# Kernel optimization log

Hardware: AMD Instinct MI355X
Metric: run time of the kernel (lower is better)

Reference implementation:

```python
import jax, jax.numpy as jnp
import numpy as np

H = 128  # DECODER_LAYERS[0]
LN_EPS = 1e-3  # keras LayerNormalization default epsilon


def setup_inputs() -> dict:
    key = jax.random.key(0)
    ks = jax.random.split(key, 12)
    N_POS, N_COL, D = 1024, 512, 128
    n_seq = 8
    s = 1.0 / np.sqrt(D)
    h = 1.0 / np.sqrt(H)
    return {
        "seq_feat": jax.random.normal(ks[0], (N_POS, D), jnp.float32),
        "col_feat": jax.random.normal(ks[1], (N_COL, D), jnp.float32),
        "sequence_lengths": jnp.full((n_seq,), N_POS // n_seq, dtype=jnp.int32),
        "Ws": jax.random.normal(ks[2], (D, H), jnp.float32) * s,
        "bs": jnp.zeros((H,), jnp.float32),
        "Wc": jax.random.normal(ks[3], (D, H), jnp.float32) * s,
        "bc": jnp.zeros((H,), jnp.float32),
        "Wm": jax.random.normal(ks[4], (H, H), jnp.float32) * h,
        "bm": jnp.zeros((H,), jnp.float32),
        "gamma": jnp.ones((H,), jnp.float32),
        "beta": jnp.zeros((H,), jnp.float32),
        "Wo": jax.random.normal(ks[5], (H, 1), jnp.float32) * h,
        "bo": jnp.zeros((1,), jnp.float32),
    }


def reference(seq_feat, col_feat, sequence_lengths, Ws, bs, Wc, bc, Wm, bm, gamma, beta, Wo, bo):
    N_POS = seq_feat.shape[0]
    N_COL = col_feat.shape[0]
    n_seq = sequence_lengths.shape[0]

    seq_dec = jax.nn.relu(seq_feat @ Ws + bs)   # [N_pos, H]
    col_dec = jax.nn.relu(col_feat @ Wc + bc)   # [N_col, H]

    # broadcast outer-sum: [N_pos, N_col, H]
    logits = seq_dec[:, None, :] + col_dec[None, :, :]

    # MLP([128]): single Dense (no activation) + LayerNorm
    hmid = logits @ Wm + bm
    mu = jnp.mean(hmid, axis=-1, keepdims=True)
    var = jnp.mean(jnp.square(hmid - mu), axis=-1, keepdims=True)
    hln = (hmid - mu) / jnp.sqrt(var + LN_EPS) * gamma + beta

    raw = (hln @ Wo + bo)[..., 0]               # [N_pos, N_col]
    exp_logits = jnp.exp(raw)

    # column-axis normalization (softmax over last axis)
    M_c = exp_logits / jnp.sum(exp_logits, axis=-1, keepdims=True)

    # segment-ragged normalization over positions, per sequence
    segment_ids = jnp.repeat(jnp.arange(n_seq, dtype=jnp.int32), sequence_lengths,
                             total_repeat_length=N_POS)
    seg = jax.ops.segment_sum(exp_logits, segment_ids, num_segments=n_seq)  # [n_seq, N_col]
    M_s = exp_logits / seg[segment_ids]

    return M_c + M_s - M_c * M_s
```

## Files before the change

### kernel.cpp

```cpp
#include <hip/hip_runtime.h>

#define HDIM 128
#define NPOS 1024
#define NCOL 512
#define LN_EPS 1e-3f


__device__ __forceinline__ int seg_of(int i, const int* __restrict__ lens, int n_seq) {
    int cum = 0;
    for (int s = 0; s < n_seq; ++s) {
        cum += lens[s];
        if (i < cum) return s;
    }
    return n_seq - 1;
}

extern "C" __global__ void __launch_bounds__(256)
k1_precompute(const float* __restrict__ seq_feat, const float* __restrict__ col_feat,
              const float* __restrict__ Ws, const float* __restrict__ bsv,
              const float* __restrict__ Wc, const float* __restrict__ bcv,
              const float* __restrict__ Wm, const float* __restrict__ bmv,
              const float* __restrict__ gam, const float* __restrict__ Wo,
              float* __restrict__ AcT, float* __restrict__ BcT,
              float* __restrict__ p_arr, float* __restrict__ v_arr,
              float* __restrict__ q_arr, float* __restrict__ w_arr,
              float* __restrict__ sums, int n_seq)
{
    __shared__ float xs[8][HDIM];
    __shared__ float ds[8][HDIM];
    __shared__ float red[256];
    __shared__ float mus[8];

    const int t  = threadIdx.x;
    const int h  = t & (HDIM - 1);
    const int rh = t >> 7;
    const int b  = blockIdx.x;

    {
        int idx = b * 256 + t;
        if (idx < NPOS + n_seq * NCOL) sums[idx] = 0.f;
    }

    const bool  is_seq = (b < NPOS / 8);
    const int   i0 = (is_seq ? b : (b - NPOS / 8)) * 8;
    const float* X  = is_seq ? seq_feat : col_feat;
    const float* W1 = is_seq ? Ws : Wc;
    const float* b1 = is_seq ? bsv : bcv;

    #pragma unroll
    for (int u = 0; u < 4; ++u) {
        int fid = t + 256 * u;
        int r = fid >> 7, k = fid & (HDIM - 1);
        xs[r][k] = X[(i0 + r) * HDIM + k];
    }
    __syncthreads();

    const int rbase = rh * 4;

    {
        float bb = b1[h];
        float d0 = bb, d1 = bb, d2 = bb, d3 = bb;
        for (int k = 0; k < HDIM; k += 4) {
            float4 x0 = *(const float4*)&xs[rbase + 0][k];
            float4 x1 = *(const float4*)&xs[rbase + 1][k];
            float4 x2 = *(const float4*)&xs[rbase + 2][k];
            float4 x3 = *(const float4*)&xs[rbase + 3][k];
            float w0 = W1[(k + 0) * HDIM + h];
            float w1 = W1[(k + 1) * HDIM + h];
            float w2 = W1[(k + 2) * HDIM + h];
            float w3 = W1[(k + 3) * HDIM + h];
            d0 += x0.x * w0 + x0.y * w1 + x0.z * w2 + x0.w * w3;
            d1 += x1.x * w0 + x1.y * w1 + x1.z * w2 + x1.w * w3;
            d2 += x2.x * w0 + x2.y * w1 + x2.z * w2 + x2.w * w3;
            d3 += x3.x * w0 + x3.y * w1 + x3.z * w2 + x3.w * w3;
        }
        ds[rbase + 0][h] = fmaxf(d0, 0.f);
        ds[rbase + 1][h] = fmaxf(d1, 0.f);
        ds[rbase + 2][h] = fmaxf(d2, 0.f);
        ds[rbase + 3][h] = fmaxf(d3, 0.f);
    }
    __syncthreads();

    float aa0, aa1, aa2, aa3;
    {
        float bb = is_seq ? 0.f : bmv[h];
        aa0 = bb; aa1 = bb; aa2 = bb; aa3 = bb;
        for (int k = 0; k < HDIM; k += 4) {
            float4 x0 = *(const float4*)&ds[rbase + 0][k];
            float4 x1 = *(const float4*)&ds[rbase + 1][k];
            float4 x2 = *(const float4*)&ds[rbase + 2][k];
            float4 x3 = *(const float4*)&ds[rbase + 3][k];
            float w0 = Wm[(k + 0) * HDIM + h];
            float w1 = Wm[(k + 1) * HDIM + h];
            float w2 = Wm[(k + 2) * HDIM + h];
            float w3 = Wm[(k + 3) * HDIM + h];
            aa0 += x0.x * w0 + x0.y * w1 + x0.z * w2 + x0.w * w3;
            aa1 += x1.x * w0 + x1.y * w1 + x1.z * w2 + x1.w * w3;
            aa2 += x2.x * w0 + x2.y * w1 + x2.z * w2 + x2.w * w3;
            aa3 += x3.x * w0 + x3.y * w1 + x3.z * w2 + x3.w * w3;
        }
    }

    xs[rbase + 0][h] = aa0;
    xs[rbase + 1][h] = aa1;
    xs[rbase + 2][h] = aa2;
    xs[rbase + 3][h] = aa3;
    __syncthreads();
    {
        int r = t >> 5, l = t & 31;
        red[t] = xs[r][l] + xs[r][l + 32] + xs[r][l + 64] + xs[r][l + 96];
    }
    __syncthreads();
    if (t < 8) {
        float s = 0.f;
        #pragma unroll
        for (int m = 0; m < 32; ++m) s += red[t * 32 + m];
        mus[t] = s * (1.f / HDIM);
    }
    __syncthreads();

    const float gw = gam[h] * Wo[h];
    float a0 = aa0 - mus[rbase + 0];
    float a1 = aa1 - mus[rbase + 1];
    float a2 = aa2 - mus[rbase + 2];
    float a3 = aa3 - mus[rbase + 3];

    {
        float4 st = make_float4(a0, a1, a2, a3);
        if (is_seq) *(float4*)&AcT[h * NPOS + i0 + rbase] = st;
        else        *(float4*)&BcT[h * NCOL + i0 + rbase] = st;
    }

    xs[rbase + 0][h] = a0 * gw;
    xs[rbase + 1][h] = a1 * gw;
    xs[rbase + 2][h] = a2 * gw;
    xs[rbase + 3][h] = a3 * gw;
    __syncthreads();
    {
        int r = t >> 5, l = t & 31;
        red[t] = xs[r][l] + xs[r][l + 32] + xs[r][l + 64] + xs[r][l + 96];
    }
    __syncthreads();
    if (t < 8) {
        float s = 0.f;
        #pragma unroll
        for (int m = 0; m < 32; ++m) s += red[t * 32 + m];
        (is_seq ? p_arr : q_arr)[i0 + t] = s;
    }
    __syncthreads();

    xs[rbase + 0][h] = a0 * a0;
    xs[rbase + 1][h] = a1 * a1;
    xs[rbase + 2][h] = a2 * a2;
    xs[rbase + 3][h] = a3 * a3;
    __syncthreads();
    {
        int r = t >> 5, l = t & 31;
        red[t] = xs[r][l] + xs[r][l + 32] + xs[r][l + 64] + xs[r][l + 96];
    }
    __syncthreads();
    if (t < 8) {
        float s = 0.f;
        #pragma unroll
        for (int m = 0; m < 32; ++m) s += red[t * 32 + m];
        (is_seq ? v_arr : w_arr)[i0 + t] = s * (1.f / HDIM);
    }
}

#define AS_STR 36
#define BS_STR 68

extern "C" __global__ void __launch_bounds__(256)
k2_gemm(const float* __restrict__ AcT, const float* __restrict__ BcT,
        const float* __restrict__ p_arr, const float* __restrict__ v_arr,
        const float* __restrict__ q_arr, const float* __restrict__ w_arr,
        const int* __restrict__ lens, int n_seq,
        float* __restrict__ E, float* __restrict__ rowsum, float* __restrict__ segsum)
{
    __shared__ float As[128 * AS_STR];
    __shared__ float Bs[128 * BS_STR];
    __shared__ float redr[512];
    __shared__ float redc[1024];

    const int t  = threadIdx.x;
    const int tc = t & 15;
    const int tr = t >> 4;
    const int i0 = blockIdx.x * 32;
    const int j0 = blockIdx.y * 64;

    #pragma unroll
    for (int u = 0; u < 4; ++u) {
        int fid = t + 256 * u;
        int k = fid >> 3, m4 = fid & 7;
        float4 g = *(const float4*)&AcT[k * NPOS + i0 + 4 * m4];
        *(float4*)&As[k * AS_STR + 4 * m4] = g;
    }
    #pragma unroll
    for (int u = 0; u < 8; ++u) {
        int fid = t + 256 * u;
        int k = fid >> 4, n4 = fid & 15;
        float4 g = *(const float4*)&BcT[k * NCOL + j0 + 4 * n4];
        *(float4*)&Bs[k * BS_STR + 4 * n4] = g;
    }
    __syncthreads();

    float acc00 = 0.f, acc01 = 0.f, acc02 = 0.f, acc03 = 0.f;
    float acc10 = 0.f, acc11 = 0.f, acc12 = 0.f, acc13 = 0.f;
    #pragma unroll 4
    for (int k = 0; k < 128; ++k) {
        float2 a2 = *(const float2*)&As[k * AS_STR + 2 * tr];
        float4 b4 = *(const float4*)&Bs[k * BS_STR + 4 * tc];
        acc00 += a2.x * b4.x; acc01 += a2.x * b4.y; acc02 += a2.x * b4.z; acc03 += a2.x * b4.w;
        acc10 += a2.y * b4.x; acc11 += a2.y * b4.y; acc12 += a2.y * b4.z; acc13 += a2.y * b4.w;
    }

    const int jj = j0 + 4 * tc;
    float4 q4 = *(const float4*)&q_arr[jj];
    float4 w4 = *(const float4*)&w_arr[jj];

    float e[2][4];
    float rs[2];
    #pragma unroll
    for (int mm = 0; mm < 2; ++mm) {
        const int i = i0 + 2 * tr + mm;
        const float pi = p_arr[i];
        const float vi = v_arr[i];
        float d0 = (mm == 0) ? acc00 : acc10;
        float d1 = (mm == 0) ? acc01 : acc11;
        float d2 = (mm == 0) ? acc02 : acc12;
        float d3 = (mm == 0) ? acc03 : acc13;
        e[mm][0] = __expf((pi + q4.x) * rsqrtf(vi + w4.x + d0 * (2.f / HDIM) + LN_EPS));
        e[mm][1] = __expf((pi + q4.y) * rsqrtf(vi + w4.y + d1 * (2.f / HDIM) + LN_EPS));
        e[mm][2] = __expf((pi + q4.z) * rsqrtf(vi + w4.z + d2 * (2.f / HDIM) + LN_EPS));
        e[mm][3] = __expf((pi + q4.w) * rsqrtf(vi + w4.w + d3 * (2.f / HDIM) + LN_EPS));
        rs[mm] = e[mm][0] + e[mm][1] + e[mm][2] + e[mm][3];
        float4 st = make_float4(e[mm][0], e[mm][1], e[mm][2], e[mm][3]);
        *(float4*)&E[i * NCOL + jj] = st;
    }

    redr[(2 * tr + 0) * 16 + tc] = rs[0];
    redr[(2 * tr + 1) * 16 + tc] = rs[1];
    #pragma unroll
    for (int u = 0; u < 4; ++u)
        redc[(4 * tc + u) * 16 + tr] = e[0][u] + e[1][u];

    const int seg_lo = seg_of(i0, lens, n_seq);
    const int seg_hi = seg_of(i0 + 31, lens, n_seq);
    __syncthreads();

    if (t < 32) {
        float s = 0.f;
        #pragma unroll
        for (int m = 0; m < 16; ++m) s += redr[t * 16 + m];
        atomicAdd(&rowsum[i0 + t], s);
    } else if (t < 96 && seg_lo == seg_hi) {
        int c = t - 32;
        float s = 0.f;
        #pragma unroll
        for (int m = 0; m < 16; ++m) s += redc[c * 16 + m];
        atomicAdd(&segsum[seg_lo * NCOL + j0 + c], s);
    }
    if (seg_lo != seg_hi) {
        #pragma unroll
        for (int mm = 0; mm < 2; ++mm) {
            const int i = i0 + 2 * tr + mm;
            const int sg = seg_of(i, lens, n_seq);
            #pragma unroll
            for (int u = 0; u < 4; ++u)
                atomicAdd(&segsum[sg * NCOL + jj + u], e[mm][u]);
        }
    }
}

extern "C" __global__ void __launch_bounds__(256)
k3_final(const float* __restrict__ E, const float* __restrict__ rowsum,
         const float* __restrict__ segsum, const int* __restrict__ lens, int n_seq,
         float* __restrict__ out)
{
    const int gid = blockIdx.x * 256 + threadIdx.x;
    const int i = gid >> 7;
    const int j = (gid & 127) * 4;

    float4 e4 = *(const float4*)&E[i * NCOL + j];
    const float invr = 1.f / rowsum[i];
    const int sg = seg_of(i, lens, n_seq);
    float4 s4 = *(const float4*)&segsum[sg * NCOL + j];

    float4 o;
    {
        float mc = e4.x * invr, ms = e4.x / s4.x; o.x = mc + ms - mc * ms;
    }
    {
        float mc = e4.y * invr, ms = e4.y / s4.y; o.y = mc + ms - mc * ms;
    }
    {
        float mc = e4.z * invr, ms = e4.z / s4.z; o.z = mc + ms - mc * ms;
    }
    {
        float mc = e4.w * invr, ms = e4.w / s4.w; o.w = mc + ms - mc * ms;
    }
    *(float4*)&out[i * NCOL + j] = o;
}

extern "C" void kernel_launch(void* const* d_in, const int* in_sizes, int n_in,
                              void* d_out, int out_size, void* d_ws, size_t ws_size,
                              hipStream_t stream) {
    const float* seq_feat = (const float*)d_in[0];
    const float* col_feat = (const float*)d_in[1];
    const int*   lens     = (const int*)d_in[2];
    const float* Ws   = (const float*)d_in[3];
    const float* bs   = (const float*)d_in[4];
    const float* Wc   = (const float*)d_in[5];
    const float* bc   = (const float*)d_in[6];
    const float* Wm   = (const float*)d_in[7];
    const float* bm   = (const float*)d_in[8];
    const float* gam  = (const float*)d_in[9];
    const float* Wo   = (const float*)d_in[11];
    float* out = (float*)d_out;
    const int n_seq = in_sizes[2];

    float* ws    = (float*)d_ws;
    float* AcT   = ws;
    float* BcT   = AcT + HDIM * NPOS;
    float* p     = BcT + HDIM * NCOL;
    float* v     = p + NPOS;
    float* q     = v + NPOS;
    float* w     = q + NCOL;
    float* sums  = w + NCOL;
    float* rowsum = sums;
    float* segsum = sums + NPOS;
    float* E     = segsum + n_seq * NCOL;

    hipLaunchKernelGGL(k1_precompute, dim3(NPOS / 8 + NCOL / 8), dim3(256), 0, stream,
                       seq_feat, col_feat, Ws, bs, Wc, bc, Wm, bm, gam, Wo,
                       AcT, BcT, p, v, q, w, sums, n_seq);
    hipLaunchKernelGGL(k2_gemm, dim3(NPOS / 32, NCOL / 64), dim3(256), 0, stream,
                       AcT, BcT, p, v, q, w, lens, n_seq, E, rowsum, segsum);
    hipLaunchKernelGGL(k3_final, dim3((NPOS * NCOL / 4) / 256), dim3(256), 0, stream,
                       E, rowsum, segsum, lens, n_seq, out);
}
```

Baseline: 109.0 us.

## Split-K GEMM across 512 threads, shuffle reductions, precomputed segment ids

The precompute kernel now gives each block 4 rows with 512 threads, one output per thread, and replaces the shared-memory reductions with wave shuffles. The GEMM kernel doubles its threads and splits the K dimension in two halves that are combined through a shared-memory union. A segment-id table is built once in the first kernel so the GEMM and final kernels no longer run the linear segment search. The aim is more parallelism and fewer per-element loops, in exchange for an extra sync and combine step in the GEMM.

```diff
diff --git a/kernel.cpp b/kernel.cpp
--- a/kernel.cpp
+++ b/kernel.cpp
@@ -15,266 +15,230 @@
     return n_seq - 1;
 }
 
-extern "C" __global__ void __launch_bounds__(256)
+extern "C" __global__ void __launch_bounds__(512)
 k1_precompute(const float* __restrict__ seq_feat, const float* __restrict__ col_feat,
               const float* __restrict__ Ws, const float* __restrict__ bsv,
               const float* __restrict__ Wc, const float* __restrict__ bcv,
               const float* __restrict__ Wm, const float* __restrict__ bmv,
               const float* __restrict__ gam, const float* __restrict__ Wo,
+              const int* __restrict__ lens, int n_seq,
               float* __restrict__ AcT, float* __restrict__ BcT,
               float* __restrict__ p_arr, float* __restrict__ v_arr,
               float* __restrict__ q_arr, float* __restrict__ w_arr,
-              float* __restrict__ sums, int n_seq)
+              float* __restrict__ sums, int* __restrict__ segid)
 {
-    __shared__ float xs[8][HDIM];
-    __shared__ float ds[8][HDIM];
-    __shared__ float red[256];
-    __shared__ float mus[8];
-
-    const int t  = threadIdx.x;
-    const int h  = t & (HDIM - 1);
-    const int rh = t >> 7;
-    const int b  = blockIdx.x;
-
-    {
-        int idx = b * 256 + t;
-        if (idx < NPOS + n_seq * NCOL) sums[idx] = 0.f;
-    }
-
-    const bool  is_seq = (b < NPOS / 8);
-    const int   i0 = (is_seq ? b : (b - NPOS / 8)) * 8;
+    __shared__ float xs[4][HDIM];
+    __shared__ float ds_[4][HDIM];
+    __shared__ float partm[8], partp[8], partv[8], mus[4];
+
+    const int t    = threadIdx.x;
+    const int b    = blockIdx.x;
+    const int h    = t & 127;
+    const int r    = t >> 7;
+    const int wv   = t >> 6;
+    const int lane = t & 63;
+
+    {
+        const int nsums = NPOS + n_seq * NCOL;
+        int idx = b * 512 + t;
+        if (idx < nsums) sums[idx] = 0.f;
+        int idx2 = idx - nsums;
+        if (idx2 >= 0 && idx2 < NPOS) segid[idx2] = seg_of(idx2, lens, n_seq);
+    }
+
+    const bool  is_seq = (b < NPOS / 4);
+    const int   i0 = (is_seq ? b : (b - NPOS / 4)) * 4;
     const float* X  = is_seq ? seq_feat : col_feat;
     const float* W1 = is_seq ? Ws : Wc;
     const float* b1 = is_seq ? bsv : bcv;
 
-    #pragma unroll
-    for (int u = 0; u < 4; ++u) {
-        int fid = t + 256 * u;
-        int r = fid >> 7, k = fid & (HDIM - 1);
-        xs[r][k] = X[(i0 + r) * HDIM + k];
-    }
-    __syncthreads();
-
-    const int rbase = rh * 4;
-
-    {
-        float bb = b1[h];
-        float d0 = bb, d1 = bb, d2 = bb, d3 = bb;
+    if (t < 128) {
+        int rr = t >> 5, k4 = (t & 31) * 4;
+        *(float4*)&xs[rr][k4] = *(const float4*)&X[(i0 + rr) * HDIM + k4];
+    }
+    __syncthreads();
+
+    float d;
+    {
+        float a0 = 0.f, a1 = 0.f, a2 = 0.f, a3 = 0.f;
+        #pragma unroll 8
         for (int k = 0; k < HDIM; k += 4) {
-            float4 x0 = *(const float4*)&xs[rbase + 0][k];
-            float4 x1 = *(const float4*)&xs[rbase + 1][k];
-            float4 x2 = *(const float4*)&xs[rbase + 2][k];
-            float4 x3 = *(const float4*)&xs[rbase + 3][k];
+            float4 x = *(const float4*)&xs[r][k];
             float w0 = W1[(k + 0) * HDIM + h];
             float w1 = W1[(k + 1) * HDIM + h];
             float w2 = W1[(k + 2) * HDIM + h];
             float w3 = W1[(k + 3) * HDIM + h];
-            d0 += x0.x * w0 + x0.y * w1 + x0.z * w2 + x0.w * w3;
-            d1 += x1.x * w0 + x1.y * w1 + x1.z * w2 + x1.w * w3;
-            d2 += x2.x * w0 + x2.y * w1 + x2.z * w2 + x2.w * w3;
-            d3 += x3.x * w0 + x3.y * w1 + x3.z * w2 + x3.w * w3;
-        }
-        ds[rbase + 0][h] = fmaxf(d0, 0.f);
-        ds[rbase + 1][h] = fmaxf(d1, 0.f);
-        ds[rbase + 2][h] = fmaxf(d2, 0.f);
-        ds[rbase + 3][h] = fmaxf(d3, 0.f);
-    }
-    __syncthreads();
-
-    float aa0, aa1, aa2, aa3;
-    {
-        float bb = is_seq ? 0.f : bmv[h];
-        aa0 = bb; aa1 = bb; aa2 = bb; aa3 = bb;
+            a0 += x.x * w0; a1 += x.y * w1; a2 += x.z * w2; a3 += x.w * w3;
+        }
+        d = fmaxf(b1[h] + ((a0 + a1) + (a2 + a3)), 0.f);
+    }
+    ds_[r][h] = d;
+    __syncthreads();
+
+    float aa;
+    {
+        float a0 = 0.f, a1 = 0.f, a2 = 0.f, a3 = 0.f;
+        #pragma unroll 8
         for (int k = 0; k < HDIM; k += 4) {
-            float4 x0 = *(const float4*)&ds[rbase + 0][k];
-            float4 x1 = *(const float4*)&ds[rbase + 1][k];
-            float4 x2 = *(const float4*)&ds[rbase + 2][k];
-            float4 x3 = *(const float4*)&ds[rbase + 3][k];
+            float4 x = *(const float4*)&ds_[r][k];
             float w0 = Wm[(k + 0) * HDIM + h];
             float w1 = Wm[(k + 1) * HDIM + h];
             float w2 = Wm[(k + 2) * HDIM + h];
             float w3 = Wm[(k + 3) * HDIM + h];
-            aa0 += x0.x * w0 + x0.y * w1 + x0.z * w2 + x0.w * w3;
-            aa1 += x1.x * w0 + x1.y * w1 + x1.z * w2 + x1.w * w3;
-            aa2 += x2.x * w0 + x2.y * w1 + x2.z * w2 + x2.w * w3;
-            aa3 += x3.x * w0 + x3.y * w1 + x3.z * w2 + x3.w * w3;
-        }
-    }
-
-    xs[rbase + 0][h] = aa0;
-    xs[rbase + 1][h] = aa1;
-    xs[rbase + 2][h] = aa2;
-    xs[rbase + 3][h] = aa3;
-    __syncthreads();
-    {
-        int r = t >> 5, l = t & 31;
-        red[t] = xs[r][l] + xs[r][l + 32] + xs[r][l + 64] + xs[r][l + 96];
-    }
-    __syncthreads();
-    if (t < 8) {
-        float s = 0.f;
-        #pragma unroll
-        for (int m = 0; m < 32; ++m) s += red[t * 32 + m];
-        mus[t] = s * (1.f / HDIM);
-    }
-    __syncthreads();
-
+            a0 += x.x * w0; a1 += x.y * w1; a2 += x.z * w2; a3 += x.w * w3;
+        }
+        aa = (is_seq ? 0.f : bmv[h]) + ((a0 + a1) + (a2 + a3));
+    }
+
+    {
+        float s = aa;
+        #pragma unroll
+        for (int off = 32; off; off >>= 1) s += __shfl_xor(s, off, 64);
+        if (lane == 0) partm[wv] = s;
+    }
+    __syncthreads();
+    if (t < 4) mus[t] = (partm[2 * t] + partm[2 * t + 1]) * (1.f / HDIM);
+    __syncthreads();
+
+    const float a  = aa - mus[r];
     const float gw = gam[h] * Wo[h];
-    float a0 = aa0 - mus[rbase + 0];
-    float a1 = aa1 - mus[rbase + 1];
-    float a2 = aa2 - mus[rbase + 2];
-    float a3 = aa3 - mus[rbase + 3];
-
-    {
-        float4 st = make_float4(a0, a1, a2, a3);
-        if (is_seq) *(float4*)&AcT[h * NPOS + i0 + rbase] = st;
-        else        *(float4*)&BcT[h * NCOL + i0 + rbase] = st;
-    }
-
-    xs[rbase + 0][h] = a0 * gw;
-    xs[rbase + 1][h] = a1 * gw;
-    xs[rbase + 2][h] = a2 * gw;
-    xs[rbase + 3][h] = a3 * gw;
-    __syncthreads();
-    {
-        int r = t >> 5, l = t & 31;
-        red[t] = xs[r][l] + xs[r][l + 32] + xs[r][l + 64] + xs[r][l + 96];
-    }
-    __syncthreads();
-    if (t < 8) {
-        float s = 0.f;
-        #pragma unroll
-        for (int m = 0; m < 32; ++m) s += red[t * 32 + m];
-        (is_seq ? p_arr : q_arr)[i0 + t] = s;
-    }
-    __syncthreads();
-
-    xs[rbase + 0][h] = a0 * a0;
-    xs[rbase + 1][h] = a1 * a1;
-    xs[rbase + 2][h] = a2 * a2;
-    xs[rbase + 3][h] = a3 * a3;
-    __syncthreads();
-    {
-        int r = t >> 5, l = t & 31;
-        red[t] = xs[r][l] + xs[r][l + 32] + xs[r][l + 64] + xs[r][l + 96];
-    }
-    __syncthreads();
-    if (t < 8) {
-        float s = 0.f;
-        #pragma unroll
-        for (int m = 0; m < 32; ++m) s += red[t * 32 + m];
-        (is_seq ? v_arr : w_arr)[i0 + t] = s * (1.f / HDIM);
+
+    {
+        float sp = a * gw, sv = a * a;
+        #pragma unroll
+        for (int off = 32; off; off >>= 1) {
+            sp += __shfl_xor(sp, off, 64);
+            sv += __shfl_xor(sv, off, 64);
+        }
+        if (lane == 0) { partp[wv] = sp; partv[wv] = sv; }
+    }
+    xs[r][h] = a;
+    __syncthreads();
+    if (t < 4) {
+        (is_seq ? p_arr : q_arr)[i0 + t] = partp[2 * t] + partp[2 * t + 1];
+        (is_seq ? v_arr : w_arr)[i0 + t] = (partv[2 * t] + partv[2 * t + 1]) * (1.f / HDIM);
+    }
+    if (t < 128) {
+        float4 st = make_float4(xs[0][t], xs[1][t], xs[2][t], xs[3][t]);
+        if (is_seq) *(float4*)&AcT[t * NPOS + i0] = st;
+        else        *(float4*)&BcT[t * NCOL + i0] = st;
     }
 }
 
 #define AS_STR 36
 #define BS_STR 68
 
-extern "C" __global__ void __launch_bounds__(256)
+union K2Smem {
+    struct { float As[128 * AS_STR]; float Bs[128 * BS_STR]; } s;
+    struct { float comb[8 * 256]; float redr[512]; float redc[1024]; } r;
+};
+
+extern "C" __global__ void __launch_bounds__(512)
 k2_gemm(const float* __restrict__ AcT, const float* __restrict__ BcT,
         const float* __restrict__ p_arr, const float* __restrict__ v_arr,
         const float* __restrict__ q_arr, const float* __restrict__ w_arr,
-        const int* __restrict__ lens, int n_seq,
+        const int* __restrict__ segid, int n_seq,
         float* __restrict__ E, float* __restrict__ rowsum, float* __restrict__ segsum)
 {
-    __shared__ float As[128 * AS_STR];
-    __shared__ float Bs[128 * BS_STR];
-    __shared__ float redr[512];
-    __shared__ float redc[1024];
+    __shared__ K2Smem sm;
 
     const int t  = threadIdx.x;
-    const int tc = t & 15;
-    const int tr = t >> 4;
+    const int tt = t & 255;
+    const int tc = tt & 15;
+    const int tr = tt >> 4;
+    const int kbase = (t >> 8) * 64;
     const int i0 = blockIdx.x * 32;
     const int j0 = blockIdx.y * 64;
 
     #pragma unroll
+    for (int u = 0; u < 2; ++u) {
+        int fid = t + 512 * u;
+        int k = fid >> 3, m4 = fid & 7;
+        *(float4*)&sm.s.As[k * AS_STR + 4 * m4] = *(const float4*)&AcT[k * NPOS + i0 + 4 * m4];
+    }
+    #pragma unroll
     for (int u = 0; u < 4; ++u) {
-        int fid = t + 256 * u;
-        int k = fid >> 3, m4 = fid & 7;
-        float4 g = *(const float4*)&AcT[k * NPOS + i0 + 4 * m4];
-        *(float4*)&As[k * AS_STR + 4 * m4] = g;
-    }
-    #pragma unroll
-    for (int u = 0; u < 8; ++u) {
-        int fid = t + 256 * u;
+        int fid = t + 512 * u;
         int k = fid >> 4, n4 = fid & 15;
-        float4 g = *(const float4*)&BcT[k * NCOL + j0 + 4 * n4];
-        *(float4*)&Bs[k * BS_STR + 4 * n4] = g;
-    }
-    __syncthreads();
-
-    float acc00 = 0.f, acc01 = 0.f, acc02 = 0.f, acc03 = 0.f;
-    float acc10 = 0.f, acc11 = 0.f, acc12 = 0.f, acc13 = 0.f;
+        *(float4*)&sm.s.Bs[k * BS_STR + 4 * n4] = *(const float4*)&BcT[k * NCOL + j0 + 4 * n4];
+    }
+    __syncthreads();
+
+    float acc[8] = {0.f, 0.f, 0.f, 0.f, 0.f, 0.f, 0.f, 0.f};
     #pragma unroll 4
-    for (int k = 0; k < 128; ++k) {
-        float2 a2 = *(const float2*)&As[k * AS_STR + 2 * tr];
-        float4 b4 = *(const float4*)&Bs[k * BS_STR + 4 * tc];
-        acc00 += a2.x * b4.x; acc01 += a2.x * b4.y; acc02 += a2.x * b4.z; acc03 += a2.x * b4.w;
-        acc10 += a2.y * b4.x; acc11 += a2.y * b4.y; acc12 += a2.y * b4.z; acc13 += a2.y * b4.w;
-    }
-
-    const int jj = j0 + 4 * tc;
-    float4 q4 = *(const float4*)&q_arr[jj];
-    float4 w4 = *(const float4*)&w_arr[jj];
+    for (int k = kbase; k < kbase + 64; ++k) {
+        float2 a2 = *(const float2*)&sm.s.As[k * AS_STR + 2 * tr];
+        float4 b4 = *(const float4*)&sm.s.Bs[k * BS_STR + 4 * tc];
+        acc[0] += a2.x * b4.x; acc[1] += a2.x * b4.y; acc[2] += a2.x * b4.z; acc[3] += a2.x * b4.w;
+        acc[4] += a2.y * b4.x; acc[5] += a2.y * b4.y; acc[6] += a2.y * b4.z; acc[7] += a2.y * b4.w;
+    }
+
+    const int seg_lo = segid[i0];
+    const int seg_hi = segid[i0 + 31];
+    __syncthreads();
+
+    if (t >= 256) {
+        #pragma unroll
+        for (int j = 0; j < 8; ++j) sm.r.comb[j * 256 + tt] = acc[j];
+    }
+    __syncthreads();
 
     float e[2][4];
-    float rs[2];
-    #pragma unroll
-    for (int mm = 0; mm < 2; ++mm) {
-        const int i = i0 + 2 * tr + mm;
-        const float pi = p_arr[i];
-        const float vi = v_arr[i];
-        float d0 = (mm == 0) ? acc00 : acc10;
-        float d1 = (mm == 0) ? acc01 : acc11;
-        float d2 = (mm == 0) ? acc02 : acc12;
-        float d3 = (mm == 0) ? acc03 : acc13;
-        e[mm][0] = __expf((pi + q4.x) * rsqrtf(vi + w4.x + d0 * (2.f / HDIM) + LN_EPS));
-        e[mm][1] = __expf((pi + q4.y) * rsqrtf(vi + w4.y + d1 * (2.f / HDIM) + LN_EPS));
-        e[mm][2] = __expf((pi + q4.z) * rsqrtf(vi + w4.z + d2 * (2.f / HDIM) + LN_EPS));
-        e[mm][3] = __expf((pi + q4.w) * rsqrtf(vi + w4.w + d3 * (2.f / HDIM) + LN_EPS));
-        rs[mm] = e[mm][0] + e[mm][1] + e[mm][2] + e[mm][3];
-        float4 st = make_float4(e[mm][0], e[mm][1], e[mm][2], e[mm][3]);
-        *(float4*)&E[i * NCOL + jj] = st;
-    }
-
-    redr[(2 * tr + 0) * 16 + tc] = rs[0];
-    redr[(2 * tr + 1) * 16 + tc] = rs[1];
-    #pragma unroll
-    for (int u = 0; u < 4; ++u)
-        redc[(4 * tc + u) * 16 + tr] = e[0][u] + e[1][u];
-
-    const int seg_lo = seg_of(i0, lens, n_seq);
-    const int seg_hi = seg_of(i0 + 31, lens, n_seq);
+    if (t < 256) {
+        #pragma unroll
+        for (int j = 0; j < 8; ++j) acc[j] += sm.r.comb[j * 256 + tt];
+
+        const int jj = j0 + 4 * tc;
+        float4 q4 = *(const float4*)&q_arr[jj];
+        float4 w4 = *(const float4*)&w_arr[jj];
+        float rs[2];
+        #pragma unroll
+        for (int mm = 0; mm < 2; ++mm) {
+            const int i = i0 + 2 * tr + mm;
+            const float pi = p_arr[i];
+            const float vi = v_arr[i];
+            e[mm][0] = __expf((pi + q4.x) * rsqrtf(vi + w4.x + acc[4*mm+0] * (2.f/HDIM) + LN_EPS));
+            e[mm][1] = __expf((pi + q4.y) * rsqrtf(vi + w4.y + acc[4*mm+1] * (2.f/HDIM) + LN_EPS));
+            e[mm][2] = __expf((pi + q4.z) * rsqrtf(vi + w4.z + acc[4*mm+2] * (2.f/HDIM) + LN_EPS));
+            e[mm][3] = __expf((pi + q4.w) * rsqrtf(vi + w4.w + acc[4*mm+3] * (2.f/HDIM) + LN_EPS));
+            rs[mm] = e[mm][0] + e[mm][1] + e[mm][2] + e[mm][3];
+            *(float4*)&E[i * NCOL + jj] = make_float4(e[mm][0], e[mm][1], e[mm][2], e[mm][3]);
+        }
+        sm.r.redr[(2 * tr + 0) * 16 + tc] = rs[0];
+        sm.r.redr[(2 * tr + 1) * 16 + tc] = rs[1];
+        #pragma unroll
+        for (int u = 0; u < 4; ++u)
+            sm.r.redc[(4 * tc + u) * 16 + tr] = e[0][u] + e[1][u];
+    }
     __syncthreads();
 
     if (t < 32) {
         float s = 0.f;
         #pragma unroll
-        for (int m = 0; m < 16; ++m) s += redr[t * 16 + m];
+        for (int m = 0; m < 16; ++m) s += sm.r.redr[t * 16 + m];
         atomicAdd(&rowsum[i0 + t], s);
-    } else if (t < 96 && seg_lo == seg_hi) {
+    } else if (t >= 32 && t < 96 && seg_lo == seg_hi) {
         int c = t - 32;
         float s = 0.f;
         #pragma unroll
-        for (int m = 0; m < 16; ++m) s += redc[c * 16 + m];
+        for (int m = 0; m < 16; ++m) s += sm.r.redc[c * 16 + m];
         atomicAdd(&segsum[seg_lo * NCOL + j0 + c], s);
     }
-    if (seg_lo != seg_hi) {
+    if (seg_lo != seg_hi && t < 256) {
         #pragma unroll
         for (int mm = 0; mm < 2; ++mm) {
             const int i = i0 + 2 * tr + mm;
-            const int sg = seg_of(i, lens, n_seq);
+            const int sg = segid[i];
             #pragma unroll
             for (int u = 0; u < 4; ++u)
-                atomicAdd(&segsum[sg * NCOL + jj + u], e[mm][u]);
+                atomicAdd(&segsum[sg * NCOL + j0 + 4 * tc + u], e[mm][u]);
         }
     }
 }
 
 extern "C" __global__ void __launch_bounds__(256)
 k3_final(const float* __restrict__ E, const float* __restrict__ rowsum,
-         const float* __restrict__ segsum, const int* __restrict__ lens, int n_seq,
+         const float* __restrict__ segsum, const int* __restrict__ segid,
          float* __restrict__ out)
 {
     const int gid = blockIdx.x * 256 + threadIdx.x;
@@ -283,22 +247,14 @@
 
     float4 e4 = *(const float4*)&E[i * NCOL + j];
     const float invr = 1.f / rowsum[i];
-    const int sg = seg_of(i, lens, n_seq);
+    const int sg = segid[i];
     float4 s4 = *(const float4*)&segsum[sg * NCOL + j];
 
     float4 o;
-    {
-        float mc = e4.x * invr, ms = e4.x / s4.x; o.x = mc + ms - mc * ms;
-    }
-    {
-        float mc = e4.y * invr, ms = e4.y / s4.y; o.y = mc + ms - mc * ms;
-    }
-    {
-        float mc = e4.z * invr, ms = e4.z / s4.z; o.z = mc + ms - mc * ms;
-    }
-    {
-        float mc = e4.w * invr, ms = e4.w / s4.w; o.w = mc + ms - mc * ms;
-    }
+    { float mc = e4.x * invr, ms = e4.x / s4.x; o.x = mc + ms - mc * ms; }
+    { float mc = e4.y * invr, ms = e4.y / s4.y; o.y = mc + ms - mc * ms; }
+    { float mc = e4.z * invr, ms = e4.z / s4.z; o.z = mc + ms - mc * ms; }
+    { float mc = e4.w * invr, ms = e4.w / s4.w; o.w = mc + ms - mc * ms; }
     *(float4*)&out[i * NCOL + j] = o;
 }
 
@@ -319,23 +275,24 @@
     float* out = (float*)d_out;
     const int n_seq = in_sizes[2];
 
-    float* ws    = (float*)d_ws;
-    float* AcT   = ws;
-    float* BcT   = AcT + HDIM * NPOS;
-    float* p     = BcT + HDIM * NCOL;
-    float* v     = p + NPOS;
-    float* q     = v + NPOS;
-    float* w     = q + NCOL;
-    float* sums  = w + NCOL;
+    float* ws     = (float*)d_ws;
+    float* AcT    = ws;
+    float* BcT    = AcT + HDIM * NPOS;
+    float* p      = BcT + HDIM * NCOL;
+    float* v      = p + NPOS;
+    float* q      = v + NPOS;
+    float* w      = q + NCOL;
+    float* sums   = w + NCOL;
     float* rowsum = sums;
     float* segsum = sums + NPOS;
-    float* E     = segsum + n_seq * NCOL;
-
-    hipLaunchKernelGGL(k1_precompute, dim3(NPOS / 8 + NCOL / 8), dim3(256), 0, stream,
+    float* E      = segsum + n_seq * NCOL;
+    int*   segid  = (int*)(E + NPOS * NCOL);
+
+    hipLaunchKernelGGL(k1_precompute, dim3(NPOS / 4 + NCOL / 4), dim3(512), 0, stream,
                        seq_feat, col_feat, Ws, bs, Wc, bc, Wm, bm, gam, Wo,
-                       AcT, BcT, p, v, q, w, sums, n_seq);
-    hipLaunchKernelGGL(k2_gemm, dim3(NPOS / 32, NCOL / 64), dim3(256), 0, stream,
-                       AcT, BcT, p, v, q, w, lens, n_seq, E, rowsum, segsum);
+                       lens, n_seq, AcT, BcT, p, v, q, w, sums, segid);
+    hipLaunchKernelGGL(k2_gemm, dim3(NPOS / 32, NCOL / 64), dim3(512), 0, stream,
+                       AcT, BcT, p, v, q, w, segid, n_seq, E, rowsum, segsum);
     hipLaunchKernelGGL(k3_final, dim3((NPOS * NCOL / 4) / 256), dim3(256), 0, stream,
-                       E, rowsum, segsum, lens, n_seq, out);
-}
+                       E, rowsum, segsum, segid, out);
+}
```

Result: faster. 100.9 us (-7.4%).
